# Kernel tuning notes

Measured on AMD Instinct MI355X. Metric: run time of the kernel, lower is better.

## Reference

```python
import jax, jax.numpy as jnp
import numpy as np

SR = 44100
B, T = 4, SR * 3          # batch, samples (duration_secs=3)
NWT, L = 64, 512          # n_wavetables, wavetable_len


def setup_inputs() -> dict:
    key = jax.random.key(0)
    k1, k2, k3, k4, k5 = jax.random.split(key, 5)
    pitch = jax.random.uniform(k1, (B, T, 1), dtype=jnp.float32, minval=50.0, maxval=500.0)
    amplitude = jax.random.uniform(k2, (B, T, 1), dtype=jnp.float32)
    y = jax.random.normal(k3, (B, T), dtype=jnp.float32)
    wavetables = jax.random.normal(k4, (NWT, L), dtype=jnp.float32) * 0.01
    # replicate init: last sample equals first sample of each table
    wavetables = wavetables.at[:, -1].set(wavetables[:, 0])
    conv_w = jax.random.normal(k5, (1, 1, 5), dtype=jnp.float32) * 0.3  # Conv1d(1,1,5)
    conv_b = jnp.zeros((1,), dtype=jnp.float32)
    return {"pitch": pitch, "amplitude": amplitude, "y": y,
            "wavetables": wavetables, "conv_w": conv_w, "conv_b": conv_b,
            "duration_secs": 3}


def reference(pitch, amplitude, y, wavetables, conv_w, conv_b, duration_secs):
    Lwt = wavetables.shape[1]
    freq = pitch.squeeze(-1)                                   # (B, T)
    increment = freq / SR * Lwt                                # (B, T)
    # NOTE: faithful to source: subtract batch-row 0 from every row
    index = jnp.cumsum(increment, axis=1) - increment[0]
    index = index % Lwt
    idx_low = jnp.floor(index)
    idx_high = jnp.ceil(index)
    alpha = index - idx_low                                    # (B, T)
    il = idx_low.astype(jnp.int32)
    ih = idx_high.astype(jnp.int32) % Lwt
    # vectorized over all 64 wavetables at once (source loops in Python)
    low = jnp.take(wavetables, il, axis=1)                     # (N, B, T)
    high = jnp.take(wavetables, ih, axis=1)                    # (N, B, T)
    waveforms = low + alpha * (high - low)                     # (N, B, T)
    # attention: mean over batch of waveform * y
    att = jnp.mean(waveforms * y, axis=1)                      # (N, T)
    att = jax.lax.conv_general_dilated(
        att[:, None, :], conv_w, window_strides=(1,), padding=[(2, 2)],
        dimension_numbers=("NCH", "OIH", "NCH"))[:, 0, :] + conv_b[0]
    att = jax.nn.softmax(att, axis=0)                          # softmax over wavetables
    out = jnp.einsum("nbt,nt->bt", waveforms, att)             # (B, T)
    out = out[..., None] * amplitude                           # (B, T, 1)
    return out
```

## Files before the change

kernel.cpp:

```cpp
#include <hip/hip_runtime.h>
#include <math.h>

#define LWT 512
#define NWT 64
#define BB 4
#define SBASE 16


#define INC_C ((float)(512.0 / 44100.0))

__device__ __forceinline__ float inc_mul(float p) {
  float v = p * INC_C;
  asm volatile("" : "+v"(v));
  return v;
}
__device__ __forceinline__ float inc_of(const float* p, int t) { return inc_mul(p[t]); }

__global__ void __launch_bounds__(256) scan_level0(const float* __restrict__ pitch,
                                                   float* __restrict__ sarr,
                                                   float* __restrict__ s1g,
                                                   int T, int NB1) {
  int k = blockIdx.x * blockDim.x + threadIdx.x;
  int b = blockIdx.y;
  if (k >= NB1) return;
  const float* prow = pitch + (size_t)b * T;
  float* srow = sarr + (size_t)b * T;
  int t0 = k * SBASE;
  float run = 0.0f;
  if (t0 + SBASE <= T) {
    const float4* p4 = reinterpret_cast<const float4*>(prow + t0);
    float4* s4o = reinterpret_cast<float4*>(srow + t0);
#pragma unroll
    for (int i = 0; i < 4; ++i) {
      float4 v = p4[i];
      float4 o;
      run += inc_mul(v.x); o.x = run;
      run += inc_mul(v.y); o.y = run;
      run += inc_mul(v.z); o.z = run;
      run += inc_mul(v.w); o.w = run;
      s4o[i] = o;
    }
  } else {
    for (int t = t0; t < T; ++t) { run += inc_of(prow, t); srow[t] = run; }
  }
  s1g[(size_t)b * NB1 + k] = run;
}

__global__ void __launch_bounds__(1024) scan_upper(float* __restrict__ s1g, int NB1) {
  int b = blockIdx.x;
  int tid = threadIdx.x;
  float* s1r = s1g + (size_t)b * NB1;
  __shared__ float s1[8320];
  __shared__ float s2[544];
  __shared__ float s3[48];
  __shared__ float s4[16];
  const int NB2 = (NB1 + SBASE - 1) / SBASE;
  const int NB3 = (NB2 + SBASE - 1) / SBASE;
  const int NB4 = (NB3 + SBASE - 1) / SBASE;

  for (int a = tid; a < NB1; a += 1024) s1[a] = s1r[a];
  __syncthreads();
  for (int k = tid; k < NB2; k += 1024) {
    int a0 = k * SBASE, a1 = a0 + SBASE < NB1 ? a0 + SBASE : NB1;
    float run = 0.0f;
    for (int a = a0; a < a1; ++a) { run += s1[a]; s1[a] = run; }
    s2[k] = run;
  }
  __syncthreads();
  for (int k = tid; k < NB3; k += 1024) {
    int a0 = k * SBASE, a1 = a0 + SBASE < NB2 ? a0 + SBASE : NB2;
    float run = 0.0f;
    for (int a = a0; a < a1; ++a) { run += s2[a]; s2[a] = run; }
    s3[k] = run;
  }
  __syncthreads();
  for (int k = tid; k < NB4; k += 1024) {
    int a0 = k * SBASE, a1 = a0 + SBASE < NB3 ? a0 + SBASE : NB3;
    float run = 0.0f;
    for (int a = a0; a < a1; ++a) { run += s3[a]; s3[a] = run; }
    s4[k] = run;
  }
  __syncthreads();
  if (tid == 0) { float r = 0.0f; for (int a = 0; a < NB4; ++a) { r += s4[a]; s4[a] = r; } }
  __syncthreads();
  for (int a = tid; a < NB3; a += 1024)
    if (a >= SBASE) s3[a] = s3[a] + s4[a / SBASE - 1];
  __syncthreads();
  for (int a = tid; a < NB2; a += 1024)
    if (a >= SBASE) s2[a] = s2[a] + s3[a / SBASE - 1];
  __syncthreads();
  for (int a = tid; a < NB1; a += 1024) {
    float v = s1[a];
    if (a >= SBASE) v = v + s2[a / SBASE - 1];
    s1r[a] = v;
  }
}

__global__ void transpose_wt(const float* __restrict__ wt, float* __restrict__ wtT) {
  int i = blockIdx.x * blockDim.x + threadIdx.x;
  if (i < NWT * LWT) {
    int n = i >> 9, c = i & 511;
    wtT[c * NWT + n] = wt[i];
  }
}

__device__ __forceinline__ float dpp_reduce_add(float x) {
  x += __int_as_float(__builtin_amdgcn_update_dpp(0, __float_as_int(x), 0xB1, 0xf, 0xf, true));
  x += __int_as_float(__builtin_amdgcn_update_dpp(0, __float_as_int(x), 0x4E, 0xf, 0xf, true));
  x += __int_as_float(__builtin_amdgcn_update_dpp(0, __float_as_int(x), 0x141, 0xf, 0xf, true));
  x += __int_as_float(__builtin_amdgcn_update_dpp(0, __float_as_int(x), 0x140, 0xf, 0xf, true));
  x += __int_as_float(__builtin_amdgcn_update_dpp(0, __float_as_int(x), 0x142, 0xa, 0xf, true));
  x += __int_as_float(__builtin_amdgcn_update_dpp(0, __float_as_int(x), 0x143, 0xc, 0xf, true));
  return __int_as_float(__builtin_amdgcn_readlane(__float_as_int(x), 63));
}

__global__ void __launch_bounds__(256) fused_out(
    const float* __restrict__ pitch, const float* __restrict__ sarr,
    const float* __restrict__ s1g, const float* __restrict__ y,
    const float* __restrict__ amp, const float* __restrict__ wtT,
    const float* __restrict__ cw, const float* __restrict__ cb,
    float* __restrict__ out, int T, int NB1) {
  __shared__ float lds_att[68][64];
  __shared__ uint2 lds_stage[68][4];
  __shared__ float y_lds[68][4];
  __shared__ float amp_lds[68][4];
  __shared__ float out_lds[4][64];
  int t0 = blockIdx.x * 64;
  int wid = threadIdx.x >> 6, lane = threadIdx.x & 63;

  {
    int b = wid;
    for (int i = lane; i < 68; i += 64) {
      int t = t0 - 2 + i;
      if (t >= 0 && t < T) {
        float S = sarr[(size_t)b * T + t];
        if (t >= SBASE) S = S + s1g[b * NB1 + (t >> 4) - 1];
        float iv = S - inc_of(pitch, t);
        float q = iv * (1.0f / 512.0f);
        float k = floorf(q);
        iv = fmaf(-k, 512.0f, iv);
        float fl = floorf(iv);
        float alpha = iv - fl;
        int ili = (int)fl; if (ili > 511) ili = 511;
        int ihi = ((int)ceilf(iv)) & 511;
        uint2 st;
        st.x = (unsigned)ili | ((unsigned)ihi << 16);
        st.y = __float_as_uint(alpha);
        lds_stage[i][b] = st;
        y_lds[i][b] = y[(size_t)b * T + t];
        amp_lds[i][b] = amp[(size_t)b * T + t];
      }
    }
  }
  __syncthreads();

  for (int i = wid; i < 68; i += 4) {
    int t = t0 - 2 + i;
    float acc = 0.0f;
    if (t >= 0 && t < T) {
      const float4 yv = *reinterpret_cast<const float4*>(&y_lds[i][0]);
#pragma unroll
      for (int b = 0; b < BB; ++b) {
        uint2 st = lds_stage[i][b];
        int ili = st.x & 0xffff, ihi = st.x >> 16;
        float alpha = __uint_as_float(st.y);
        float lo = wtT[ili * NWT + lane];
        float hi = wtT[ihi * NWT + lane];
        float yb = b == 0 ? yv.x : b == 1 ? yv.y : b == 2 ? yv.z : yv.w;
        acc += (lo + alpha * (hi - lo)) * yb;
      }
      acc *= 0.25f;
    }
    lds_att[i][lane] = acc;
  }
  __syncthreads();

  float w0 = cw[0], w1 = cw[1], w2 = cw[2], w3 = cw[3], w4 = cw[4];
  float bias = cb[0];
#pragma unroll 4
  for (int i = wid; i < 64; i += 4) {
    int t = t0 + i;
    if (t >= T) continue;
    float c = bias + lds_att[i][lane] * w0 + lds_att[i + 1][lane] * w1 +
              lds_att[i + 2][lane] * w2 + lds_att[i + 3][lane] * w3 +
              lds_att[i + 4][lane] * w4;
    float e = __expf(c);
    float r0, r1, r2, r3;
    {
      uint2 st = lds_stage[i + 2][0];
      int ili = st.x & 0xffff, ihi = st.x >> 16;
      float alpha = __uint_as_float(st.y);
      float lo = wtT[ili * NWT + lane], hi = wtT[ihi * NWT + lane];
      r0 = e * (lo + alpha * (hi - lo));
    }
    {
      uint2 st = lds_stage[i + 2][1];
      int ili = st.x & 0xffff, ihi = st.x >> 16;
      float alpha = __uint_as_float(st.y);
      float lo = wtT[ili * NWT + lane], hi = wtT[ihi * NWT + lane];
      r1 = e * (lo + alpha * (hi - lo));
    }
    {
      uint2 st = lds_stage[i + 2][2];
      int ili = st.x & 0xffff, ihi = st.x >> 16;
      float alpha = __uint_as_float(st.y);
      float lo = wtT[ili * NWT + lane], hi = wtT[ihi * NWT + lane];
      r2 = e * (lo + alpha * (hi - lo));
    }
    {
      uint2 st = lds_stage[i + 2][3];
      int ili = st.x & 0xffff, ihi = st.x >> 16;
      float alpha = __uint_as_float(st.y);
      float lo = wtT[ili * NWT + lane], hi = wtT[ihi * NWT + lane];
      r3 = e * (lo + alpha * (hi - lo));
    }
    float s0 = dpp_reduce_add(r0);
    float s1_ = dpp_reduce_add(r1);
    float s2_ = dpp_reduce_add(r2);
    float s3_ = dpp_reduce_add(r3);
    float ssum = dpp_reduce_add(e);
#if __has_builtin(__builtin_amdgcn_rcpf)
    float rc = __builtin_amdgcn_rcpf(ssum);
#else
    float rc = 1.0f / ssum;
#endif
    if (lane < BB) {
      float pv = lane == 0 ? s0 : lane == 1 ? s1_ : lane == 2 ? s2_ : s3_;
      out_lds[lane][i] = pv * rc * amp_lds[i + 2][lane];
    }
  }
  __syncthreads();

  {
    int b = wid;
    int t = t0 + lane;
    if (t < T) out[(size_t)b * T + t] = out_lds[b][lane];
  }
}

extern "C" void kernel_launch(void* const* d_in, const int* in_sizes, int n_in,
                              void* d_out, int out_size, void* d_ws, size_t ws_size,
                              hipStream_t stream) {
  const float* pitch = (const float*)d_in[0];
  const float* amp   = (const float*)d_in[1];
  const float* y     = (const float*)d_in[2];
  const float* wt    = (const float*)d_in[3];
  const float* cw    = (const float*)d_in[4];
  const float* cb    = (const float*)d_in[5];
  float* out = (float*)d_out;

  int BT = in_sizes[2];
  int T = BT / BB;
  int NB1 = (T + SBASE - 1) / SBASE;

  float* ws   = (float*)d_ws;
  float* sarr = ws;
  float* wtT  = ws + (size_t)BT;
  float* s1g  = ws + (size_t)BT + NWT * LWT;

  hipLaunchKernelGGL(scan_level0, dim3((NB1 + 255) / 256, BB), dim3(256), 0, stream,
                     pitch, sarr, s1g, T, NB1);
  hipLaunchKernelGGL(scan_upper, dim3(BB), dim3(1024), 0, stream, s1g, NB1);
  hipLaunchKernelGGL(transpose_wt, dim3((NWT * LWT + 255) / 256), dim3(256), 0, stream, wt, wtT);
  hipLaunchKernelGGL(fused_out, dim3((T + 63) / 64), dim3(256), 0, stream,
                     pitch, sarr, s1g, y, amp, wtT, cw, cb, out, T, NB1);
}
```

Before: 61.79 us.

## Fold wavetable transpose into scan kernel and widen fused output tiles

The wavetable transpose becomes an extra blockIdx.y slice of the level-0 scan kernel, which removes one kernel launch. The fused output kernel now handles 128 timesteps per block with 512 threads instead of 64 with 256, so the 4-sample conv halo is a smaller share of the recomputed attention work. Staging data in LDS moves from interleaved uint2 and float4 structs to per-batch arrays. Larger blocks use more LDS and cut the block count, which may lower occupancy or load balance.

```diff
diff --git a/kernel.cpp b/kernel.cpp
--- a/kernel.cpp
+++ b/kernel.cpp
@@ -5,6 +5,8 @@
 #define NWT 64
 #define BB 4
 #define SBASE 16
+#define BLK 128
+#define HALO 132
 
 
 #define INC_C ((float)(512.0 / 44100.0))
@@ -19,7 +21,17 @@
 __global__ void __launch_bounds__(256) scan_level0(const float* __restrict__ pitch,
                                                    float* __restrict__ sarr,
                                                    float* __restrict__ s1g,
+                                                   const float* __restrict__ wt,
+                                                   float* __restrict__ wtT,
                                                    int T, int NB1) {
+  if (blockIdx.y == BB) {
+    int i = blockIdx.x * blockDim.x + threadIdx.x;
+    if (i < NWT * LWT) {
+      int n = i >> 9, c = i & 511;
+      wtT[c * NWT + n] = wt[i];
+    }
+    return;
+  }
   int k = blockIdx.x * blockDim.x + threadIdx.x;
   int b = blockIdx.y;
   if (k >= NB1) return;
@@ -96,14 +108,6 @@
   }
 }
 
-__global__ void transpose_wt(const float* __restrict__ wt, float* __restrict__ wtT) {
-  int i = blockIdx.x * blockDim.x + threadIdx.x;
-  if (i < NWT * LWT) {
-    int n = i >> 9, c = i & 511;
-    wtT[c * NWT + n] = wt[i];
-  }
-}
-
 __device__ __forceinline__ float dpp_reduce_add(float x) {
   x += __int_as_float(__builtin_amdgcn_update_dpp(0, __float_as_int(x), 0xB1, 0xf, 0xf, true));
   x += __int_as_float(__builtin_amdgcn_update_dpp(0, __float_as_int(x), 0x4E, 0xf, 0xf, true));
@@ -114,23 +118,24 @@
   return __int_as_float(__builtin_amdgcn_readlane(__float_as_int(x), 63));
 }
 
-__global__ void __launch_bounds__(256) fused_out(
+__global__ void __launch_bounds__(512) fused_out(
     const float* __restrict__ pitch, const float* __restrict__ sarr,
     const float* __restrict__ s1g, const float* __restrict__ y,
     const float* __restrict__ amp, const float* __restrict__ wtT,
     const float* __restrict__ cw, const float* __restrict__ cb,
     float* __restrict__ out, int T, int NB1) {
-  __shared__ float lds_att[68][64];
-  __shared__ uint2 lds_stage[68][4];
-  __shared__ float y_lds[68][4];
-  __shared__ float amp_lds[68][4];
-  __shared__ float out_lds[4][64];
-  int t0 = blockIdx.x * 64;
+  __shared__ float lds_att[HALO][64];
+  __shared__ unsigned ilh_l[BB][HALO];
+  __shared__ float alf_l[BB][HALO];
+  __shared__ float y_l[BB][HALO];
+  __shared__ float amp_l[BB][HALO];
+  __shared__ float out_l[BB][BLK];
+  int t0 = blockIdx.x * BLK;
   int wid = threadIdx.x >> 6, lane = threadIdx.x & 63;
 
   {
-    int b = wid;
-    for (int i = lane; i < 68; i += 64) {
+    int b = wid & 3;
+    for (int i = (wid >> 2) * 64 + lane; i < HALO; i += 128) {
       int t = t0 - 2 + i;
       if (t >= 0 && t < T) {
         float S = sarr[(size_t)b * T + t];
@@ -143,31 +148,27 @@
         float alpha = iv - fl;
         int ili = (int)fl; if (ili > 511) ili = 511;
         int ihi = ((int)ceilf(iv)) & 511;
-        uint2 st;
-        st.x = (unsigned)ili | ((unsigned)ihi << 16);
-        st.y = __float_as_uint(alpha);
-        lds_stage[i][b] = st;
-        y_lds[i][b] = y[(size_t)b * T + t];
-        amp_lds[i][b] = amp[(size_t)b * T + t];
+        ilh_l[b][i] = (unsigned)ili | ((unsigned)ihi << 16);
+        alf_l[b][i] = alpha;
+        y_l[b][i] = y[(size_t)b * T + t];
+        amp_l[b][i] = amp[(size_t)b * T + t];
       }
     }
   }
   __syncthreads();
 
-  for (int i = wid; i < 68; i += 4) {
+  for (int i = wid; i < HALO; i += 8) {
     int t = t0 - 2 + i;
     float acc = 0.0f;
     if (t >= 0 && t < T) {
-      const float4 yv = *reinterpret_cast<const float4*>(&y_lds[i][0]);
 #pragma unroll
       for (int b = 0; b < BB; ++b) {
-        uint2 st = lds_stage[i][b];
-        int ili = st.x & 0xffff, ihi = st.x >> 16;
-        float alpha = __uint_as_float(st.y);
+        unsigned st = ilh_l[b][i];
+        int ili = st & 0xffff, ihi = st >> 16;
+        float alpha = alf_l[b][i];
         float lo = wtT[ili * NWT + lane];
         float hi = wtT[ihi * NWT + lane];
-        float yb = b == 0 ? yv.x : b == 1 ? yv.y : b == 2 ? yv.z : yv.w;
-        acc += (lo + alpha * (hi - lo)) * yb;
+        acc += (lo + alpha * (hi - lo)) * y_l[b][i];
       }
       acc *= 0.25f;
     }
@@ -178,7 +179,7 @@
   float w0 = cw[0], w1 = cw[1], w2 = cw[2], w3 = cw[3], w4 = cw[4];
   float bias = cb[0];
 #pragma unroll 4
-  for (int i = wid; i < 64; i += 4) {
+  for (int i = wid; i < BLK; i += 8) {
     int t = t0 + i;
     if (t >= T) continue;
     float c = bias + lds_att[i][lane] * w0 + lds_att[i + 1][lane] * w1 +
@@ -187,31 +188,27 @@
     float e = __expf(c);
     float r0, r1, r2, r3;
     {
-      uint2 st = lds_stage[i + 2][0];
-      int ili = st.x & 0xffff, ihi = st.x >> 16;
-      float alpha = __uint_as_float(st.y);
-      float lo = wtT[ili * NWT + lane], hi = wtT[ihi * NWT + lane];
+      unsigned st = ilh_l[0][i + 2];
+      float alpha = alf_l[0][i + 2];
+      float lo = wtT[(st & 0xffff) * NWT + lane], hi = wtT[(st >> 16) * NWT + lane];
       r0 = e * (lo + alpha * (hi - lo));
     }
     {
-      uint2 st = lds_stage[i + 2][1];
-      int ili = st.x & 0xffff, ihi = st.x >> 16;
-      float alpha = __uint_as_float(st.y);
-      float lo = wtT[ili * NWT + lane], hi = wtT[ihi * NWT + lane];
+      unsigned st = ilh_l[1][i + 2];
+      float alpha = alf_l[1][i + 2];
+      float lo = wtT[(st & 0xffff) * NWT + lane], hi = wtT[(st >> 16) * NWT + lane];
       r1 = e * (lo + alpha * (hi - lo));
     }
     {
-      uint2 st = lds_stage[i + 2][2];
-      int ili = st.x & 0xffff, ihi = st.x >> 16;
-      float alpha = __uint_as_float(st.y);
-      float lo = wtT[ili * NWT + lane], hi = wtT[ihi * NWT + lane];
+      unsigned st = ilh_l[2][i + 2];
+      float alpha = alf_l[2][i + 2];
+      float lo = wtT[(st & 0xffff) * NWT + lane], hi = wtT[(st >> 16) * NWT + lane];
       r2 = e * (lo + alpha * (hi - lo));
     }
     {
-      uint2 st = lds_stage[i + 2][3];
-      int ili = st.x & 0xffff, ihi = st.x >> 16;
-      float alpha = __uint_as_float(st.y);
-      float lo = wtT[ili * NWT + lane], hi = wtT[ihi * NWT + lane];
+      unsigned st = ilh_l[3][i + 2];
+      float alpha = alf_l[3][i + 2];
+      float lo = wtT[(st & 0xffff) * NWT + lane], hi = wtT[(st >> 16) * NWT + lane];
       r3 = e * (lo + alpha * (hi - lo));
     }
     float s0 = dpp_reduce_add(r0);
@@ -226,15 +223,15 @@
 #endif
     if (lane < BB) {
       float pv = lane == 0 ? s0 : lane == 1 ? s1_ : lane == 2 ? s2_ : s3_;
-      out_lds[lane][i] = pv * rc * amp_lds[i + 2][lane];
+      out_l[lane][i] = pv * rc * amp_l[lane][i + 2];
     }
   }
   __syncthreads();
 
   {
-    int b = wid;
-    int t = t0 + lane;
-    if (t < T) out[(size_t)b * T + t] = out_lds[b][lane];
+    int b = threadIdx.x >> 7, toff = threadIdx.x & 127;
+    int t = t0 + toff;
+    if (t < T) out[(size_t)b * T + t] = out_l[b][toff];
   }
 }
 
@@ -258,10 +255,9 @@
   float* wtT  = ws + (size_t)BT;
   float* s1g  = ws + (size_t)BT + NWT * LWT;
 
-  hipLaunchKernelGGL(scan_level0, dim3((NB1 + 255) / 256, BB), dim3(256), 0, stream,
-                     pitch, sarr, s1g, T, NB1);
+  hipLaunchKernelGGL(scan_level0, dim3(128, BB + 1), dim3(256), 0, stream,
+                     pitch, sarr, s1g, wt, wtT, T, NB1);
   hipLaunchKernelGGL(scan_upper, dim3(BB), dim3(1024), 0, stream, s1g, NB1);
-  hipLaunchKernelGGL(transpose_wt, dim3((NWT * LWT + 255) / 256), dim3(256), 0, stream, wt, wtT);
-  hipLaunchKernelGGL(fused_out, dim3((T + 63) / 64), dim3(256), 0, stream,
+  hipLaunchKernelGGL(fused_out, dim3((T + BLK - 1) / BLK), dim3(512), 0, stream,
                      pitch, sarr, s1g, y, amp, wtT, cw, cb, out, T, NB1);
 }
```

After: 64.37 us. 4.2% more time.
